# Optimization experiments

Hardware: AMD Instinct MI355X
Metric: run time of the kernel (lower is better)

## Reference

```python
import jax, jax.numpy as jnp
import numpy as np

EMBD_D = 384
HEAD_SIZE = 64  # 384 // 6


def setup_inputs() -> dict:
    key = jax.random.key(0)
    kx, kq, kk, kv = jax.random.split(key, 4)
    B, T = 16, 2048
    x = jax.random.normal(kx, (B, T, EMBD_D), dtype=jnp.float32)
    s = 1.0 / np.sqrt(EMBD_D)
    Wq = jax.random.normal(kq, (EMBD_D, HEAD_SIZE), dtype=jnp.float32) * s
    Wk = jax.random.normal(kk, (EMBD_D, HEAD_SIZE), dtype=jnp.float32) * s
    Wv = jax.random.normal(kv, (EMBD_D, HEAD_SIZE), dtype=jnp.float32) * s
    return {"x": x, "Wq": Wq, "Wk": Wk, "Wv": Wv}


def reference(x, Wq, Wk, Wv):
    # x: [B,T,C]; projections to head_size=64 (Linear, no bias)
    q = jnp.einsum("btc,cd->btd", x, Wq)
    k = jnp.einsum("btc,cd->btd", x, Wk)
    v = jnp.einsum("btc,cd->btd", x, Wv)
    scale = jnp.asarray(HEAD_SIZE, q.dtype) ** -0.5
    qk = jnp.einsum("btd,bsd->bts", q, k) * scale  # [B,T,T]
    # Faithful to original quirk: tril then mask exact zeros to -inf
    masked = jnp.tril(qk)
    masked = jnp.where(masked == 0, -jnp.inf, masked)
    scores = jax.nn.softmax(masked, axis=-1)
    # dropout is identity in eval mode (reference baseline)
    return jnp.einsum("bts,bsd->btd", scores, v)
```

## Files before the change

### kernel.cpp

```cpp
#include <hip/hip_runtime.h>

typedef short bf16x8 __attribute__((ext_vector_type(8)));
typedef float f32x4 __attribute__((ext_vector_type(4)));
typedef unsigned int u32;
typedef __attribute__((address_space(1))) const u32 gu32;
typedef __attribute__((address_space(3))) u32 lu32;

#define NEG_INF (-__builtin_inff())

static __device__ __forceinline__ unsigned short f2bf(float f) {
  union { float f; unsigned u; } v; v.f = f;
  return (unsigned short)((v.u + 0x7fffu + ((v.u >> 16) & 1u)) >> 16);
}
static __device__ __forceinline__ unsigned fbits(float f) {
  union { float f; unsigned u; } v; v.f = f;
  return v.u;
}
static __device__ __forceinline__ unsigned pack2(float a, float b) {
  return __builtin_amdgcn_perm(fbits(b) + 0x8000u, fbits(a) + 0x8000u, 0x07060302u);
}
static __device__ __forceinline__ f32x4 mfma16(bf16x8 a, bf16x8 b, f32x4 c) {
  return __builtin_amdgcn_mfma_f32_16x16x32_bf16(a, b, c, 0, 0, 0);
}
static __device__ __forceinline__ void dma16(const void* g, void* l) {
  __builtin_amdgcn_global_load_lds((gu32*)g, (lu32*)l, 16, 0, 0);
}

__global__ __launch_bounds__(256) void prep_w(const float* __restrict__ wq,
                                              const float* __restrict__ wk,
                                              const float* __restrict__ wv,
                                              char* __restrict__ wt) {
  int i = blockIdx.x * 256 + threadIdx.x;
  if (i >= 384 * 64) return;
  int c = i >> 6, d = i & 63;
  int c6 = c >> 6, cin = c & 63;
  const float Cs = 0.18033688011112042f;
  long base = (long)(c6 * 192) * 128;
  int col = (cin * 2) ^ ((d & 7) << 4);
  *(unsigned short*)(wt + base + (long)d * 128 + col) = f2bf(wq[i] * Cs);
  *(unsigned short*)(wt + base + (long)(64 + d) * 128 + col) = f2bf(wk[i]);
  *(unsigned short*)(wt + base + (long)(128 + d) * 128 + col) = f2bf(wv[i]);
}

__global__ __launch_bounds__(256, 2) void proj_kernel(
    const float* __restrict__ x, const char* __restrict__ wt,
    unsigned short* __restrict__ qo, char* __restrict__ kT,
    char* __restrict__ vT) {
  __shared__ char wls[2][24576];
  const int tid = threadIdx.x;
  const int wave = tid >> 6, lane = tid & 63;
  const int lo = lane & 15, quad = lane >> 4;
  const long tok0 = ((long)blockIdx.x * 4 + wave) * 16;

#pragma unroll
  for (int s2 = 0; s2 < 6; ++s2) {
    const int s = wave * 6 + s2;
    dma16(wt + s * 1024 + lane * 16, &wls[0][s * 1024]);
  }
  bf16x8 ax[12];
  const float* xr = x + (tok0 + lo) * 384 + quad * 8;
#pragma unroll
  for (int kk = 0; kk < 12; ++kk) {
    float4 x0 = *(const float4*)(xr + kk * 32);
    float4 x1 = *(const float4*)(xr + kk * 32 + 4);
    bf16x8 a;
    a[0] = (short)f2bf(x0.x); a[1] = (short)f2bf(x0.y);
    a[2] = (short)f2bf(x0.z); a[3] = (short)f2bf(x0.w);
    a[4] = (short)f2bf(x1.x); a[5] = (short)f2bf(x1.y);
    a[6] = (short)f2bf(x1.z); a[7] = (short)f2bf(x1.w);
    ax[kk] = a;
  }

  f32x4 acc[12];
#pragma unroll
  for (int nt = 0; nt < 12; ++nt) acc[nt] = (f32x4){0.f, 0.f, 0.f, 0.f};

  for (int c6 = 0; c6 < 6; ++c6) {
    const int buf = c6 & 1;
    __syncthreads();
    if (c6 < 5) {
      const char* wg = wt + (long)(c6 + 1) * 24576;
#pragma unroll
      for (int s2 = 0; s2 < 6; ++s2) {
        const int s = wave * 6 + s2;
        dma16(wg + s * 1024 + lane * 16, &wls[buf ^ 1][s * 1024]);
      }
    }
#pragma unroll
    for (int kk = 0; kk < 2; ++kk) {
      const bf16x8 axk = ax[c6 * 2 + kk];
#pragma unroll
      for (int nt = 0; nt < 12; ++nt) {
        const int dd = nt * 16 + lo;
        const int col = ((kk * 4 + quad) ^ (lo & 7)) << 4;
        bf16x8 wf = *(const bf16x8*)(&wls[buf][dd * 128 + col]);
        if (nt < 8)
          acc[nt] = mfma16(wf, axk, acc[nt]);
        else
          acc[nt] = mfma16(axk, wf, acc[nt]);
      }
    }
  }

  const long bb = tok0 >> 11;
  const int tin0 = (int)(tok0 & 2047);
  const int kt = tin0 >> 6;
  const long tile = ((bb * 32 + kt) << 13);
  const int key0w = (tin0 & 63) + quad * 4;
  const int keyl = (tin0 & 63) + lo;
#pragma unroll
  for (int nt = 0; nt < 12; ++nt) {
    uint2 uu;
    uu.x = pack2(acc[nt][0], acc[nt][1]);
    uu.y = pack2(acc[nt][2], acc[nt][3]);
    if (nt < 4) {
      *(uint2*)(qo + (tok0 + lo) * 64 + nt * 16 + quad * 4) = uu;
    } else if (nt < 8) {
      const int d0 = (nt - 4) * 16 + quad * 4;
      *(uint2*)(kT + tile + keyl * 128 + (((d0 * 2) ^ ((keyl & 7) << 4)))) = uu;
    } else {
      const int d = (nt - 8) * 16 + lo;
      *(uint2*)(vT + tile + d * 128 + (((key0w * 2) ^ ((d & 7) << 4)))) = uu;
    }
  }
}

static __device__ __forceinline__ void load_tile(const char* kg, const char* vg,
                                                 int lo, int quad, int swz,
                                                 bf16x8 (&kf)[8], bf16x8 (&vf)[8]) {
#pragma unroll
  for (int t = 0; t < 4; ++t) {
    const int row = (t * 16 + lo) * 128;
    kf[2 * t] = *(const bf16x8*)(kg + row + ((quad ^ swz) << 4));
    kf[2 * t + 1] = *(const bf16x8*)(kg + row + (((4 + quad) ^ swz) << 4));
  }
#pragma unroll
  for (int kk2 = 0; kk2 < 2; ++kk2) {
#pragma unroll
    for (int dt = 0; dt < 4; ++dt) {
      const int rowv = (dt * 16 + lo) * 128;
      vf[kk2 * 4 + dt] = *(const bf16x8*)(vg + rowv + (((kk2 * 4 + quad) ^ swz) << 4));
    }
  }
}

static __device__ __forceinline__ void compute_tile(
    const bf16x8 (&kf)[8], const bf16x8 (&vf)[8], bf16x8 bq0, bf16x8 bq1,
    unsigned short* psw , int lo, int quad,
    bool diag, int key0, int qrl, f32x4 (&oacc)[4], float& l) {
#pragma unroll
  for (int t = 0; t < 4; ++t) {
    f32x4 s = (f32x4){0.f, 0.f, 0.f, 0.f};
    s = mfma16(kf[2 * t], bq0, s);
    s = mfma16(kf[2 * t + 1], bq1, s);
    if (diag) {
#pragma unroll
      for (int r = 0; r < 4; ++r)
        if (key0 + t * 16 + quad * 4 + r > qrl) s[r] = NEG_INF;
    }
    float e0 = __builtin_amdgcn_exp2f(s[0]);
    float e1 = __builtin_amdgcn_exp2f(s[1]);
    float e2 = __builtin_amdgcn_exp2f(s[2]);
    float e3 = __builtin_amdgcn_exp2f(s[3]);
    l += (e0 + e1) + (e2 + e3);
    uint2 uu;
    uu.x = pack2(e0, e1);
    uu.y = pack2(e2, e3);
    *(uint2*)(psw + lo * 72 + t * 16 + quad * 4) = uu;
  }
  asm volatile("s_waitcnt lgkmcnt(0)" ::: "memory");
#pragma unroll
  for (int kk2 = 0; kk2 < 2; ++kk2) {
    bf16x8 bp = *(const bf16x8*)(psw + lo * 72 + kk2 * 32 + quad * 8);
#pragma unroll
    for (int dt = 0; dt < 4; ++dt) {
      oacc[dt] = mfma16(vf[kk2 * 4 + dt], bp, oacc[dt]);
    }
  }
}

__global__ __launch_bounds__(256, 2) void attn_kernel(
    const unsigned short* __restrict__ qg, const char* __restrict__ kT,
    const char* __restrict__ vT, float* __restrict__ out) {
  __shared__ unsigned short ps[4][16][72];

  const int tid = threadIdx.x;
  const int h = tid >> 6, lane = tid & 63;
  const int lo = lane & 15, quad = lane >> 4;
  const int b = blockIdx.x & 15;
  const int idx = blockIdx.x >> 4;
  const int a = (blockIdx.x < 256) ? (31 - idx) : (idx - 16);
  const int j = 4 * a + h;
  const int niter = a + 1;
  const int qrow0 = j * 16;

  const unsigned short* qb = qg + (long)b * 2048 * 64;
  const char* kbT = kT + ((long)b * 32 << 13);
  const char* vbT = vT + ((long)b * 32 << 13);
  float* ob = out + (long)b * 2048 * 64;

  const unsigned short* qr = qb + (long)(qrow0 + lo) * 64 + quad * 8;
  const bf16x8 bq0 = *(const bf16x8*)qr;
  const bf16x8 bq1 = *(const bf16x8*)(qr + 32);

  f32x4 oacc[4];
#pragma unroll
  for (int dt = 0; dt < 4; ++dt) oacc[dt] = (f32x4){0.f, 0.f, 0.f, 0.f};
  float l = 0.f;
  const int swz = (lo & 7);
  const int qrl = qrow0 + lo;
  unsigned short* psw = &ps[h][0][0];

  bf16x8 kA[8], vA[8], kB[8], vB[8];
  load_tile(kbT, vbT, lo, quad, swz, kA, vA);

  int kt = 0;
  for (; kt + 2 <= niter; kt += 2) {
    load_tile(kbT + ((long)(kt + 1) << 13), vbT + ((long)(kt + 1) << 13), lo,
              quad, swz, kB, vB);
    compute_tile(kA, vA, bq0, bq1, psw, lo, quad, false, kt * 64, qrl,
                 oacc, l);
    if (kt + 2 < niter)
      load_tile(kbT + ((long)(kt + 2) << 13), vbT + ((long)(kt + 2) << 13), lo,
                quad, swz, kA, vA);
    compute_tile(kB, vB, bq0, bq1, psw, lo, quad,
                 (kt + 1 == niter - 1), (kt + 1) * 64, qrl, oacc, l);
  }
  if (kt < niter) {
    compute_tile(kA, vA, bq0, bq1, psw, lo, quad, true, kt * 64, qrl,
                 oacc, l);
  }

  l += __shfl_xor(l, 16, 64);
  l += __shfl_xor(l, 32, 64);
  const float inv = 1.0f / l;
  float* orow = ob + (long)(qrow0 + lo) * 64;
#pragma unroll
  for (int dt = 0; dt < 4; ++dt) {
    float4 st;
    st.x = oacc[dt][0] * inv; st.y = oacc[dt][1] * inv;
    st.z = oacc[dt][2] * inv; st.w = oacc[dt][3] * inv;
    *(float4*)(orow + dt * 16 + quad * 4) = st;
  }
}

extern "C" void kernel_launch(void* const* d_in, const int* in_sizes, int n_in,
                              void* d_out, int out_size, void* d_ws, size_t ws_size,
                              hipStream_t stream) {
  const float* x = (const float*)d_in[0];
  const float* wq = (const float*)d_in[1];
  const float* wk = (const float*)d_in[2];
  const float* wv = (const float*)d_in[3];
  float* out = (float*)d_out;

  char* ws = (char*)d_ws;
  char* wt = ws;
  const size_t MB4 = (size_t)4 * 1024 * 1024;
  unsigned short* qws = (unsigned short*)(ws + 147456);
  char* kT = ws + 147456 + MB4;
  char* vT = ws + 147456 + 2 * MB4;

  prep_w<<<96, 256, 0, stream>>>(wq, wk, wv, wt);
  proj_kernel<<<512, 256, 0, stream>>>(x, wt, qws, kT, vT);
  attn_kernel<<<512, 256, 0, stream>>>(qws, kT, vT, out);
}
```

Baseline: 125.2 us.

## Fuse weight prep, projection and attention into one cooperative persistent kernel

Merges the three launches (weight conversion, QKV projection, causal attention) into a single cooperative kernel that synchronises through global atomic flags. A global counter gates projection on weight conversion, and a per-batch counter gates attention on that batch's K/V tiles. Q stays in registers instead of going through a workspace round trip. The aim is to remove launch gaps and the Q global write/read. In exchange it adds a memset and spin-wait barriers, relies on all 512 blocks being co-resident, and keeps the old three-kernel path as a fallback if the cooperative launch fails.

```diff
diff --git a/kernel.cpp b/kernel.cpp
--- a/kernel.cpp
+++ b/kernel.cpp
@@ -24,6 +24,245 @@
 }
 static __device__ __forceinline__ void dma16(const void* g, void* l) {
   __builtin_amdgcn_global_load_lds((gu32*)g, (lu32*)l, 16, 0, 0);
+}
+
+static __device__ __forceinline__ void load_tile(const char* kg, const char* vg,
+                                                 int lo, int quad, int swz,
+                                                 bf16x8 (&kf)[8], bf16x8 (&vf)[8]) {
+#pragma unroll
+  for (int t = 0; t < 4; ++t) {
+    const int row = (t * 16 + lo) * 128;
+    kf[2 * t] = *(const bf16x8*)(kg + row + ((quad ^ swz) << 4));
+    kf[2 * t + 1] = *(const bf16x8*)(kg + row + (((4 + quad) ^ swz) << 4));
+  }
+#pragma unroll
+  for (int kk2 = 0; kk2 < 2; ++kk2) {
+#pragma unroll
+    for (int dt = 0; dt < 4; ++dt) {
+      const int rowv = (dt * 16 + lo) * 128;
+      vf[kk2 * 4 + dt] = *(const bf16x8*)(vg + rowv + (((kk2 * 4 + quad) ^ swz) << 4));
+    }
+  }
+}
+
+static __device__ __forceinline__ void compute_tile(
+    const bf16x8 (&kf)[8], const bf16x8 (&vf)[8], bf16x8 bq0, bf16x8 bq1,
+    unsigned short* psw , int lo, int quad,
+    bool diag, int key0, int qrl, f32x4 (&oacc)[4], float& l) {
+#pragma unroll
+  for (int t = 0; t < 4; ++t) {
+    f32x4 s = (f32x4){0.f, 0.f, 0.f, 0.f};
+    s = mfma16(kf[2 * t], bq0, s);
+    s = mfma16(kf[2 * t + 1], bq1, s);
+    if (diag) {
+#pragma unroll
+      for (int r = 0; r < 4; ++r)
+        if (key0 + t * 16 + quad * 4 + r > qrl) s[r] = NEG_INF;
+    }
+    float e0 = __builtin_amdgcn_exp2f(s[0]);
+    float e1 = __builtin_amdgcn_exp2f(s[1]);
+    float e2 = __builtin_amdgcn_exp2f(s[2]);
+    float e3 = __builtin_amdgcn_exp2f(s[3]);
+    l += (e0 + e1) + (e2 + e3);
+    uint2 uu;
+    uu.x = pack2(e0, e1);
+    uu.y = pack2(e2, e3);
+    *(uint2*)(psw + lo * 72 + t * 16 + quad * 4) = uu;
+  }
+  asm volatile("s_waitcnt lgkmcnt(0)" ::: "memory");
+#pragma unroll
+  for (int kk2 = 0; kk2 < 2; ++kk2) {
+    bf16x8 bp = *(const bf16x8*)(psw + lo * 72 + kk2 * 32 + quad * 8);
+#pragma unroll
+    for (int dt = 0; dt < 4; ++dt) {
+      oacc[dt] = mfma16(vf[kk2 * 4 + dt], bp, oacc[dt]);
+    }
+  }
+}
+
+__global__ __launch_bounds__(256, 2) void fused_kernel(
+    const float* __restrict__ x, const float* __restrict__ wq,
+    const float* __restrict__ wk, const float* __restrict__ wv,
+    char* __restrict__ wt, char* __restrict__ kT, char* __restrict__ vT,
+    u32* __restrict__ flags, float* __restrict__ out) {
+  __shared__ __align__(16) union {
+    char wls[2][24576];
+    unsigned short ps[4][16][72];
+  } sm;
+
+  const int tid = threadIdx.x;
+  const int bid = blockIdx.x;
+  const int wave = tid >> 6, lane = tid & 63;
+  const int lo = lane & 15, quad = lane >> 4;
+
+  const int b = bid & 15;
+  const int idx = bid >> 4;
+  const int g = (bid < 256) ? (31 - idx) : (idx - 16);
+  const long tok0 = (long)b * 2048 + g * 64 + wave * 16;
+
+  if (bid < 96) {
+    const int i = bid * 256 + tid;
+    const int c = i >> 6, d = i & 63;
+    const int c6 = c >> 6, cin = c & 63;
+    const float Cs = 0.18033688011112042f;
+    const long base = (long)(c6 * 192) * 128;
+    const int col = (cin * 2) ^ ((d & 7) << 4);
+    *(unsigned short*)(wt + base + (long)d * 128 + col) = f2bf(wq[i] * Cs);
+    *(unsigned short*)(wt + base + (long)(64 + d) * 128 + col) = f2bf(wk[i]);
+    *(unsigned short*)(wt + base + (long)(128 + d) * 128 + col) = f2bf(wv[i]);
+  }
+
+  bf16x8 ax[12];
+  {
+    const float* xr = x + (tok0 + lo) * 384 + quad * 8;
+#pragma unroll
+    for (int kk = 0; kk < 12; ++kk) {
+      float4 x0 = *(const float4*)(xr + kk * 32);
+      float4 x1 = *(const float4*)(xr + kk * 32 + 4);
+      bf16x8 a2;
+      a2[0] = (short)f2bf(x0.x); a2[1] = (short)f2bf(x0.y);
+      a2[2] = (short)f2bf(x0.z); a2[3] = (short)f2bf(x0.w);
+      a2[4] = (short)f2bf(x1.x); a2[5] = (short)f2bf(x1.y);
+      a2[6] = (short)f2bf(x1.z); a2[7] = (short)f2bf(x1.w);
+      ax[kk] = a2;
+    }
+  }
+
+  __syncthreads();
+  if (tid == 0) {
+    if (bid < 96) {
+      __threadfence();
+      atomicAdd(&flags[0], 1u);
+    }
+    while (__hip_atomic_load(&flags[0], __ATOMIC_ACQUIRE,
+                             __HIP_MEMORY_SCOPE_AGENT) < 96u)
+      __builtin_amdgcn_s_sleep(8);
+  }
+  __syncthreads();
+
+  uint2 qu[4];
+  {
+#pragma unroll
+    for (int s2 = 0; s2 < 6; ++s2) {
+      const int s = wave * 6 + s2;
+      dma16(wt + s * 1024 + lane * 16, &sm.wls[0][s * 1024]);
+    }
+    f32x4 acc[12];
+#pragma unroll
+    for (int nt = 0; nt < 12; ++nt) acc[nt] = (f32x4){0.f, 0.f, 0.f, 0.f};
+
+    for (int c6 = 0; c6 < 6; ++c6) {
+      const int buf = c6 & 1;
+      __syncthreads();
+      if (c6 < 5) {
+        const char* wg = wt + (long)(c6 + 1) * 24576;
+#pragma unroll
+        for (int s2 = 0; s2 < 6; ++s2) {
+          const int s = wave * 6 + s2;
+          dma16(wg + s * 1024 + lane * 16, &sm.wls[buf ^ 1][s * 1024]);
+        }
+      }
+#pragma unroll
+      for (int kk = 0; kk < 2; ++kk) {
+        const bf16x8 axk = ax[c6 * 2 + kk];
+#pragma unroll
+        for (int nt = 0; nt < 12; ++nt) {
+          const int dd = nt * 16 + lo;
+          const int col = ((kk * 4 + quad) ^ (lo & 7)) << 4;
+          bf16x8 wf = *(const bf16x8*)(&sm.wls[buf][dd * 128 + col]);
+          if (nt < 8)
+            acc[nt] = mfma16(wf, axk, acc[nt]);
+          else
+            acc[nt] = mfma16(axk, wf, acc[nt]);
+        }
+      }
+    }
+
+    const long tile = ((long)(b * 32 + g) << 13);
+    const int tin = wave * 16;
+    const int key0w = tin + quad * 4;
+    const int keyl = tin + lo;
+#pragma unroll
+    for (int nt = 0; nt < 12; ++nt) {
+      uint2 uu;
+      uu.x = pack2(acc[nt][0], acc[nt][1]);
+      uu.y = pack2(acc[nt][2], acc[nt][3]);
+      if (nt < 4) {
+        qu[nt] = uu;
+      } else if (nt < 8) {
+        const int d0 = (nt - 4) * 16 + quad * 4;
+        *(uint2*)(kT + tile + keyl * 128 + (((d0 * 2) ^ ((keyl & 7) << 4)))) = uu;
+      } else {
+        const int d = (nt - 8) * 16 + lo;
+        *(uint2*)(vT + tile + d * 128 + (((key0w * 2) ^ ((d & 7) << 4)))) = uu;
+      }
+    }
+  }
+
+  __syncthreads();
+  if (tid == 0) {
+    __threadfence();
+    atomicAdd(&flags[16 + 16 * b], 1u);
+    while (__hip_atomic_load(&flags[16 + 16 * b], __ATOMIC_ACQUIRE,
+                             __HIP_MEMORY_SCOPE_AGENT) < 32u)
+      __builtin_amdgcn_s_sleep(8);
+  }
+  __syncthreads();
+
+  {
+    const int niter = g + 1;
+    const int qrow0 = (4 * g + wave) * 16;
+    const char* kbT = kT + ((long)b * 32 << 13);
+    const char* vbT = vT + ((long)b * 32 << 13);
+    float* ob = out + (long)b * 2048 * 64;
+    unsigned short* psw = &sm.ps[wave][0][0];
+
+#pragma unroll
+    for (int nt = 0; nt < 4; ++nt)
+      *(uint2*)(psw + lo * 72 + nt * 16 + quad * 4) = qu[nt];
+    asm volatile("s_waitcnt lgkmcnt(0)" ::: "memory");
+    const bf16x8 bq0 = *(const bf16x8*)(psw + lo * 72 + quad * 8);
+    const bf16x8 bq1 = *(const bf16x8*)(psw + lo * 72 + 32 + quad * 8);
+
+    f32x4 oacc[4];
+#pragma unroll
+    for (int dt = 0; dt < 4; ++dt) oacc[dt] = (f32x4){0.f, 0.f, 0.f, 0.f};
+    float l = 0.f;
+    const int swz = (lo & 7);
+    const int qrl = qrow0 + lo;
+
+    bf16x8 kA[8], vA[8], kB[8], vB[8];
+    load_tile(kbT, vbT, lo, quad, swz, kA, vA);
+
+    int kt = 0;
+    for (; kt + 2 <= niter; kt += 2) {
+      load_tile(kbT + ((long)(kt + 1) << 13), vbT + ((long)(kt + 1) << 13), lo,
+                quad, swz, kB, vB);
+      compute_tile(kA, vA, bq0, bq1, psw, lo, quad, false, kt * 64,
+                   qrl, oacc, l);
+      if (kt + 2 < niter)
+        load_tile(kbT + ((long)(kt + 2) << 13), vbT + ((long)(kt + 2) << 13),
+                  lo, quad, swz, kA, vA);
+      compute_tile(kB, vB, bq0, bq1, psw, lo, quad,
+                   (kt + 1 == niter - 1), (kt + 1) * 64, qrl, oacc, l);
+    }
+    if (kt < niter) {
+      compute_tile(kA, vA, bq0, bq1, psw, lo, quad, true, kt * 64,
+                   qrl, oacc, l);
+    }
+
+    l += __shfl_xor(l, 16, 64);
+    l += __shfl_xor(l, 32, 64);
+    const float inv = 1.0f / l;
+    float* orow = ob + (long)(qrow0 + lo) * 64;
+#pragma unroll
+    for (int dt = 0; dt < 4; ++dt) {
+      float4 stv;
+      stv.x = oacc[dt][0] * inv; stv.y = oacc[dt][1] * inv;
+      stv.z = oacc[dt][2] * inv; stv.w = oacc[dt][3] * inv;
+      *(float4*)(orow + dt * 16 + quad * 4) = stv;
+    }
+  }
 }
 
 __global__ __launch_bounds__(256) void prep_w(const float* __restrict__ wq,
@@ -125,60 +364,6 @@
   }
 }
 
-static __device__ __forceinline__ void load_tile(const char* kg, const char* vg,
-                                                 int lo, int quad, int swz,
-                                                 bf16x8 (&kf)[8], bf16x8 (&vf)[8]) {
-#pragma unroll
-  for (int t = 0; t < 4; ++t) {
-    const int row = (t * 16 + lo) * 128;
-    kf[2 * t] = *(const bf16x8*)(kg + row + ((quad ^ swz) << 4));
-    kf[2 * t + 1] = *(const bf16x8*)(kg + row + (((4 + quad) ^ swz) << 4));
-  }
-#pragma unroll
-  for (int kk2 = 0; kk2 < 2; ++kk2) {
-#pragma unroll
-    for (int dt = 0; dt < 4; ++dt) {
-      const int rowv = (dt * 16 + lo) * 128;
-      vf[kk2 * 4 + dt] = *(const bf16x8*)(vg + rowv + (((kk2 * 4 + quad) ^ swz) << 4));
-    }
-  }
-}
-
-static __device__ __forceinline__ void compute_tile(
-    const bf16x8 (&kf)[8], const bf16x8 (&vf)[8], bf16x8 bq0, bf16x8 bq1,
-    unsigned short* psw , int lo, int quad,
-    bool diag, int key0, int qrl, f32x4 (&oacc)[4], float& l) {
-#pragma unroll
-  for (int t = 0; t < 4; ++t) {
-    f32x4 s = (f32x4){0.f, 0.f, 0.f, 0.f};
-    s = mfma16(kf[2 * t], bq0, s);
-    s = mfma16(kf[2 * t + 1], bq1, s);
-    if (diag) {
-#pragma unroll
-      for (int r = 0; r < 4; ++r)
-        if (key0 + t * 16 + quad * 4 + r > qrl) s[r] = NEG_INF;
-    }
-    float e0 = __builtin_amdgcn_exp2f(s[0]);
-    float e1 = __builtin_amdgcn_exp2f(s[1]);
-    float e2 = __builtin_amdgcn_exp2f(s[2]);
-    float e3 = __builtin_amdgcn_exp2f(s[3]);
-    l += (e0 + e1) + (e2 + e3);
-    uint2 uu;
-    uu.x = pack2(e0, e1);
-    uu.y = pack2(e2, e3);
-    *(uint2*)(psw + lo * 72 + t * 16 + quad * 4) = uu;
-  }
-  asm volatile("s_waitcnt lgkmcnt(0)" ::: "memory");
-#pragma unroll
-  for (int kk2 = 0; kk2 < 2; ++kk2) {
-    bf16x8 bp = *(const bf16x8*)(psw + lo * 72 + kk2 * 32 + quad * 8);
-#pragma unroll
-    for (int dt = 0; dt < 4; ++dt) {
-      oacc[dt] = mfma16(vf[kk2 * 4 + dt], bp, oacc[dt]);
-    }
-  }
-}
-
 __global__ __launch_bounds__(256, 2) void attn_kernel(
     const unsigned short* __restrict__ qg, const char* __restrict__ kT,
     const char* __restrict__ vT, float* __restrict__ out) {
@@ -255,12 +440,21 @@
 
   char* ws = (char*)d_ws;
   char* wt = ws;
-  const size_t MB4 = (size_t)4 * 1024 * 1024;
-  unsigned short* qws = (unsigned short*)(ws + 147456);
-  char* kT = ws + 147456 + MB4;
-  char* vT = ws + 147456 + 2 * MB4;
-
-  prep_w<<<96, 256, 0, stream>>>(wq, wk, wv, wt);
-  proj_kernel<<<512, 256, 0, stream>>>(x, wt, qws, kT, vT);
-  attn_kernel<<<512, 256, 0, stream>>>(qws, kT, vT, out);
-}
+  u32* flags = (u32*)(ws + 151552);
+  char* kT = ws + (4 << 20);
+  char* vT = ws + (8 << 20);
+
+  hipMemsetAsync(flags, 0, 2048, stream);
+
+  void* args[] = {(void*)&x,  (void*)&wq, (void*)&wk,    (void*)&wv, (void*)&wt,
+                  (void*)&kT, (void*)&vT, (void*)&flags, (void*)&out};
+  hipError_t e = hipLaunchCooperativeKernel(
+      reinterpret_cast<const void*>(&fused_kernel), dim3(512), dim3(256), args,
+      0u, stream);
+  if (e != hipSuccess) {
+    unsigned short* qws = (unsigned short*)(ws + (12 << 20));
+    prep_w<<<96, 256, 0, stream>>>(wq, wk, wv, wt);
+    proj_kernel<<<512, 256, 0, stream>>>(x, wt, qws, kT, vT);
+    attn_kernel<<<512, 256, 0, stream>>>(qws, kT, vT, out);
+  }
+}
```

Measured after the change: 212.3 us. 69.6% more time.
